# Performance work log

Hardware: AMD Instinct MI355X
Metric: run time of the kernel (lower is better)

The kernel has to match this reference:

```python
import jax, jax.numpy as jnp
import numpy as np

NUM_HEADS = 8
EPS = 1e-12  # torch F.normalize default eps


def _l2norm(t):
    # t / max(||t||_2, eps) along last axis (matches F.normalize)
    n = jnp.sqrt(jnp.sum(t * t, axis=-1, keepdims=True))
    return t / jnp.maximum(n, EPS)


def setup_inputs() -> dict:
    key = jax.random.key(0)
    k1, k2, k3 = jax.random.split(key, 3)
    B, N, C = 8, 1024, 768
    x = jax.random.normal(k1, (B, N, C), dtype=jnp.float32)
    w_qkv = jax.random.normal(k2, (C, 3 * C), dtype=jnp.float32) * 0.02
    temperature = jnp.ones((NUM_HEADS, 1, 1), dtype=jnp.float32)
    w_proj = jax.random.normal(k3, (C, C), dtype=jnp.float32) * 0.02
    b_proj = jnp.zeros((C,), dtype=jnp.float32)
    return {"x": x, "w_qkv": w_qkv, "temperature": temperature,
            "w_proj": w_proj, "b_proj": b_proj}


def reference(x, w_qkv, temperature, w_proj, b_proj):
    B, N, C = x.shape
    H = NUM_HEADS
    hd = C // H
    # qkv projection (no bias), split into q,k,v of shape [B,H,N,hd]
    qkv = (x @ w_qkv).reshape(B, N, 3, H, hd)
    qkv = jnp.transpose(qkv, (2, 0, 3, 1, 4))  # [3,B,H,N,hd]
    q, k, v = qkv[0], qkv[1], qkv[2]
    q = _l2norm(q)
    k = _l2norm(k)
    # NOTE: code (unlike canonical XCA) does NOT transpose q/k, so attn is [B,H,N,N]
    attn = jnp.einsum('bhnd,bhmd->bhnm', q, k) * temperature  # temp broadcasts over B
    attn = jax.nn.softmax(attn, axis=-1)
    out = jnp.einsum('bhnm,bhmd->bhnd', attn, v)  # [B,H,N,hd]
    out = jnp.transpose(out, (0, 2, 1, 3)).reshape(B, N, C)
    return out @ w_proj + b_proj
```

## Files before the change

kernel.cpp:

```cpp
#include <hip/hip_runtime.h>
#include <math.h>

typedef __attribute__((ext_vector_type(8))) short bf16x8;
typedef __attribute__((ext_vector_type(4))) float f32x4;
typedef unsigned short u16;
typedef unsigned int u32;


__device__ __forceinline__ u16 f2b(float f) {
  u32 u = __float_as_uint(f);
  return (u16)((u + 0x7fffu + ((u >> 16) & 1u)) >> 16);
}
__device__ __forceinline__ float b2f(u16 h) {
  return __uint_as_float(((u32)h) << 16);
}
__device__ __forceinline__ int swz(int m) { return (m ^ (m >> 2)) & 3; }

__device__ __forceinline__ void async16(const void* g, void* l) {
  __builtin_amdgcn_global_load_lds((const __attribute__((address_space(1))) u32*)g,
                                   (__attribute__((address_space(3))) u32*)l, 16, 0, 0);
}

__global__ __launch_bounds__(256) void prep_kernel(const float* __restrict__ x,
                                                   const float* __restrict__ w_qkv,
                                                   const float* __restrict__ w_proj,
                                                   u16* __restrict__ xb,
                                                   u16* __restrict__ wqkvT,
                                                   u16* __restrict__ wprojT) {
  __shared__ float t[32][33];
  const int blk = blockIdx.x;
  if (blk < 6144) {
    const int idx = blk * 256 + threadIdx.x;
    const float4 v = ((const float4*)x)[idx];
    uint2 o;
    o.x = (u32)f2b(v.x) | ((u32)f2b(v.y) << 16);
    o.y = (u32)f2b(v.z) | ((u32)f2b(v.w) << 16);
    ((uint2*)xb)[idx] = o;
    return;
  }
  const float* in; u16* out; int R, C, bx, by;
  if (blk < 6144 + 1728) {
    const int rem = blk - 6144;
    in = w_qkv; out = wqkvT; R = 768; C = 2304; bx = rem % 72; by = rem / 72;
  } else {
    const int rem = blk - 6144 - 1728;
    in = w_proj; out = wprojT; R = 768; C = 768; bx = rem % 24; by = rem / 24;
  }
  const int c0 = bx * 32, r0 = by * 32;
  const int tc = threadIdx.x & 31, tr = threadIdx.x >> 5;
#pragma unroll
  for (int j = 0; j < 4; ++j)
    t[tr + j * 8][tc] = in[(size_t)(r0 + tr + j * 8) * C + c0 + tc];
  __syncthreads();
#pragma unroll
  for (int j = 0; j < 4; ++j)
    out[(size_t)(c0 + tr + j * 8) * R + r0 + tc] = f2b(t[tc][tr + j * 8]);
}

template<int NT>
__device__ __forceinline__ void gemm_core(const u16* __restrict__ A,
                                          const u16* __restrict__ Bt,
                                          int m0, int n0, f32x4 acc[4][NT / 32]) {
  constexpr int JT = NT / 32;
  constexpr int NINST = (512 + NT * 4) / 256;
  __shared__ u16 Sm[(512 + NT * 4) * 8];
  const int tid = threadIdx.x;
  const int w = tid >> 6, lane = tid & 63;
  const int i15 = lane & 15, quad = lane >> 4;
  const int wm = (w >> 1) * 64, wn = (w & 1) * (NT / 2);
  const int sw = quad ^ swz(i15);

#pragma unroll
  for (int i = 0; i < 4; ++i)
#pragma unroll
    for (int j = 0; j < JT; ++j) acc[i][j] = (f32x4){0.f, 0.f, 0.f, 0.f};

  for (int k0 = 0; k0 < 768; k0 += 32) {
    __syncthreads();
#pragma unroll
    for (int inst = 0; inst < NINST; ++inst) {
      const int s = inst * 256 + tid;
      const u16* src;
      if (inst < 2) {
        const int m = s >> 2, e = s & 3;
        src = A + ((size_t)(m0 + m) * 768 + k0 + (e ^ swz(m)) * 8);
      } else {
        const int s2 = s - 512;
        const int n = s2 >> 2, e = s2 & 3;
        src = Bt + ((size_t)(n0 + n) * 768 + k0 + (e ^ swz(n)) * 8);
      }
      async16(src, (void*)(Sm + (size_t)(inst * 256 + w * 64) * 8));
    }
    __syncthreads();
    bf16x8 af[4], bf[JT];
#pragma unroll
    for (int i = 0; i < 4; ++i)
      af[i] = *(const bf16x8*)(Sm + ((size_t)(wm + i * 16 + i15) * 4 + sw) * 8);
#pragma unroll
    for (int j = 0; j < JT; ++j)
      bf[j] = *(const bf16x8*)(Sm + ((size_t)512 + (wn + j * 16 + i15) * 4 + sw) * 8);
#pragma unroll
    for (int i = 0; i < 4; ++i)
#pragma unroll
      for (int j = 0; j < JT; ++j)
        acc[i][j] = __builtin_amdgcn_mfma_f32_16x16x32_bf16(af[i], bf[j], acc[i][j], 0, 0, 0);
  }
}

__global__ __launch_bounds__(256, 3) void qkv_gemm_kernel(
    const u16* __restrict__ xb, const u16* __restrict__ wT,
    const float* __restrict__ temp,
    u16* __restrict__ q, u16* __restrict__ k, u16* __restrict__ vT) {
  f32x4 acc[4][6];
  const int bid = blockIdx.x;
  const int xcd = bid & 7, slot = bid >> 3;
  const int mb = xcd * 8 + slot / 12, nb = slot % 12;
  const int m0 = mb * 128, n0 = nb * 192;
  gemm_core<192>(xb, wT, m0, n0, acc);

  const int tid = threadIdx.x, w = tid >> 6, lane = tid & 63;
  const int i15 = lane & 15, quad = lane >> 4;
  const int wm = (w >> 1) * 64;
  const int three = nb >> 2;
  const int h = ((nb & 3) << 1) + (w & 1);

  if (three < 2) {
    u16* dst = three ? k : q;
    const float sc_extra = three ? 1.f : temp[h];
#pragma unroll
    for (int it = 0; it < 4; ++it) {
#pragma unroll
      for (int r = 0; r < 4; ++r) {
        float s = 0.f;
#pragma unroll
        for (int jt = 0; jt < 6; ++jt) s += acc[it][jt][r] * acc[it][jt][r];
        s += __shfl_xor(s, 1); s += __shfl_xor(s, 2);
        s += __shfl_xor(s, 4); s += __shfl_xor(s, 8);
        const float scale = sc_extra / fmaxf(sqrtf(s), 1e-12f);
        const int m = m0 + wm + it * 16 + quad * 4 + r;
        const int b = m >> 10, n = m & 1023;
        u16* rowp = dst + ((size_t)(b * 8 + h) * 1024 + n) * 96;
#pragma unroll
        for (int jt = 0; jt < 6; ++jt)
          rowp[jt * 16 + i15] = f2b(acc[it][jt][r] * scale);
      }
    }
  } else {
#pragma unroll
    for (int it = 0; it < 4; ++it) {
      const int mb4 = m0 + wm + it * 16 + quad * 4;
      const int b = mb4 >> 10, nbase = mb4 & 1023;
#pragma unroll
      for (int jt = 0; jt < 6; ++jt) {
        const int d = jt * 16 + i15;
        uint2 pk;
        pk.x = (u32)f2b(acc[it][jt][0]) | ((u32)f2b(acc[it][jt][1]) << 16);
        pk.y = (u32)f2b(acc[it][jt][2]) | ((u32)f2b(acc[it][jt][3]) << 16);
        *(uint2*)(vT + ((size_t)(b * 8 + h) * 96 + d) * 1024 + nbase) = pk;
      }
    }
  }
}

__global__ __launch_bounds__(256, 2) void attn_kernel(
    const u16* __restrict__ q, const u16* __restrict__ kk,
    const u16* __restrict__ vT, u16* __restrict__ ctx) {
  __shared__ u16 smem[20480];
  u16* KVs = smem;
  const int tid = threadIdx.x, w = tid >> 6, lane = tid & 63;
  const int i15 = lane & 15, quad = lane >> 4;
  const int xs = swz(i15);
  const int bh = blockIdx.x & 63, qbase = (blockIdx.x >> 6) * 128;
  const int b = bh >> 3, h = bh & 7;
  u16* Pw = smem + 12288 + w * 2048;

  bf16x8 qf[2][3];
#pragma unroll
  for (int rt = 0; rt < 2; ++rt) {
    const int qrow = qbase + w * 32 + rt * 16 + i15;
    const u16* qp = q + ((size_t)bh * 1024 + qrow) * 96 + quad * 8;
#pragma unroll
    for (int c = 0; c < 3; ++c) qf[rt][c] = *(const bf16x8*)(qp + c * 32);
  }

  f32x4 o[2][6];
#pragma unroll
  for (int rt = 0; rt < 2; ++rt)
#pragma unroll
    for (int dt = 0; dt < 6; ++dt) o[rt][dt] = (f32x4){0.f, 0.f, 0.f, 0.f};
  float l[2] = {0.f, 0.f};

  const int key_s = tid >> 2, qs = tid & 3;
  const int kgq = qs ^ swz(key_s);
  int vd[3], vc2[3], vgq[3];
  vd[0] = tid >> 2;                      vc2[0] = 0;
  vd[1] = (tid < 128) ? (tid >> 2) + 64 : (tid >> 2) - 32;  vc2[1] = (tid >= 128);
  vd[2] = (tid >> 2) + 32;               vc2[2] = 1;
#pragma unroll
  for (int j = 0; j < 3; ++j) vgq[j] = qs ^ swz(vd[j]);

  uint4 kreg[3], vreg[3];
#pragma unroll
  for (int j = 0; j < 3; ++j) {
    kreg[j] = *(const uint4*)(kk + ((size_t)bh * 1024 + key_s) * 96 + (j * 4 + kgq) * 8);
    vreg[j] = *(const uint4*)(vT + ((size_t)bh * 96 + vd[j]) * 1024 + vc2[j] * 32 + vgq[j] * 8);
  }

  for (int t = 0; t < 16; ++t) {
    __syncthreads();
#pragma unroll
    for (int j = 0; j < 3; ++j) {
      *(uint4*)(KVs + (size_t)(j * 256 + tid) * 8) = kreg[j];
      *(uint4*)(KVs + (size_t)(768 + j * 256 + tid) * 8) = vreg[j];
    }
    __syncthreads();
    if (t < 15) {
      const int kt0 = (t + 1) * 64;
#pragma unroll
      for (int j = 0; j < 3; ++j) {
        kreg[j] = *(const uint4*)(kk + ((size_t)bh * 1024 + kt0 + key_s) * 96 + (j * 4 + kgq) * 8);
        vreg[j] = *(const uint4*)(vT + ((size_t)bh * 96 + vd[j]) * 1024 + kt0 + vc2[j] * 32 + vgq[j] * 8);
      }
    }
#pragma unroll
    for (int kt = 0; kt < 4; ++kt) {
      bf16x8 af[3];
#pragma unroll
      for (int c = 0; c < 3; ++c)
        af[c] = *(const bf16x8*)(KVs + ((size_t)((c * 64 + kt * 16 + i15) * 4) + (quad ^ xs)) * 8);
#pragma unroll
      for (int rt = 0; rt < 2; ++rt) {
        f32x4 s = (f32x4){0.f, 0.f, 0.f, 0.f};
#pragma unroll
        for (int c = 0; c < 3; ++c)
          s = __builtin_amdgcn_mfma_f32_16x16x32_bf16(af[c], qf[rt][c], s, 0, 0, 0);
        const float e0 = __expf(s[0]), e1 = __expf(s[1]);
        const float e2 = __expf(s[2]), e3 = __expf(s[3]);
        l[rt] += (e0 + e1) + (e2 + e3);
        uint2 pk;
        pk.x = (u32)f2b(e0) | ((u32)f2b(e1) << 16);
        pk.y = (u32)f2b(e2) | ((u32)f2b(e3) << 16);
        const int pg = (kt & 1) * 2 + (quad >> 1);
        *(uint2*)(Pw + (size_t)(((kt >> 1) * 32 + rt * 16 + i15) * 4 + (pg ^ xs)) * 8
                      + (quad & 1) * 4) = pk;
      }
    }
#pragma unroll
    for (int c2 = 0; c2 < 2; ++c2) {
      bf16x8 pa[2];
#pragma unroll
      for (int rt = 0; rt < 2; ++rt)
        pa[rt] = *(const bf16x8*)(Pw + (size_t)((c2 * 32 + rt * 16 + i15) * 4 + (quad ^ xs)) * 8);
#pragma unroll
      for (int dt = 0; dt < 6; ++dt) {
        const bf16x8 vb = *(const bf16x8*)(KVs +
            ((size_t)(768 + (c2 * 96 + dt * 16 + i15) * 4) + (quad ^ xs)) * 8);
#pragma unroll
        for (int rt = 0; rt < 2; ++rt)
          o[rt][dt] = __builtin_amdgcn_mfma_f32_16x16x32_bf16(pa[rt], vb, o[rt][dt], 0, 0, 0);
      }
    }
  }

  l[0] += __shfl_xor(l[0], 16); l[0] += __shfl_xor(l[0], 32);
  l[1] += __shfl_xor(l[1], 16); l[1] += __shfl_xor(l[1], 32);
  __syncthreads();
  u16* scr = smem + w * 5120;
#pragma unroll
  for (int rt = 0; rt < 2; ++rt) {
#pragma unroll
    for (int r = 0; r < 4; ++r) {
      const float linv = 1.f / __shfl(l[rt], quad * 4 + r);
      const int row32 = rt * 16 + quad * 4 + r;
#pragma unroll
      for (int dt = 0; dt < 6; ++dt)
        scr[row32 * 104 + dt * 16 + i15] = f2b(o[rt][dt][r] * linv);
    }
  }
#pragma unroll
  for (int jj = 0; jj < 6; ++jj) {
    const int id = jj * 64 + lane;
    const int row32 = id / 12, g = id - row32 * 12;
    const int grow = b * 1024 + qbase + w * 32 + row32;
    *(uint4*)(ctx + (size_t)grow * 768 + h * 96 + g * 8) =
        *(const uint4*)(scr + row32 * 104 + g * 8);
  }
}

__global__ __launch_bounds__(256, 4) void proj_gemm_kernel(
    const u16* __restrict__ ctx, const u16* __restrict__ wT,
    const float* __restrict__ bias, float* __restrict__ out) {
  f32x4 acc[4][2];
  const int bid = blockIdx.x;
  const int xcd = bid & 7, slot = bid >> 3;
  const int mb = xcd * 8 + slot / 12, nb = slot % 12;
  const int m0 = mb * 128, n0 = nb * 64;
  gemm_core<64>(ctx, wT, m0, n0, acc);

  const int tid = threadIdx.x, w = tid >> 6, lane = tid & 63;
  const int i15 = lane & 15, quad = lane >> 4;
  const int wm = (w >> 1) * 64, wn = (w & 1) * 32;
#pragma unroll
  for (int jt = 0; jt < 2; ++jt) {
    const int c = n0 + wn + jt * 16 + i15;
    const float bb = bias[c];
#pragma unroll
    for (int it = 0; it < 4; ++it) {
#pragma unroll
      for (int r = 0; r < 4; ++r) {
        const int m = m0 + wm + it * 16 + quad * 4 + r;
        out[(size_t)m * 768 + c] = acc[it][jt][r] + bb;
      }
    }
  }
}

extern "C" void kernel_launch(void* const* d_in, const int* in_sizes, int n_in,
                              void* d_out, int out_size, void* d_ws, size_t ws_size,
                              hipStream_t stream) {
  const float* x      = (const float*)d_in[0];
  const float* w_qkv  = (const float*)d_in[1];
  const float* temp   = (const float*)d_in[2];
  const float* w_proj = (const float*)d_in[3];
  const float* b_proj = (const float*)d_in[4];

  u16* ws      = (u16*)d_ws;
  u16* xb      = ws;
  u16* wqkvT   = xb + 6291456;
  u16* qb      = wqkvT + 1769472;
  u16* kb      = qb + 6291456;
  u16* vTb     = kb + 6291456;
  u16* ctxb    = vTb + 6291456;
  u16* wprojT  = ctxb + 6291456;

  prep_kernel<<<8448, 256, 0, stream>>>(x, w_qkv, w_proj, xb, wqkvT, wprojT);
  qkv_gemm_kernel<<<768, 256, 0, stream>>>(xb, wqkvT, temp, qb, kb, vTb);
  attn_kernel<<<512, 256, 0, stream>>>(qb, kb, vTb, ctxb);
  proj_gemm_kernel<<<768, 256, 0, stream>>>(ctxb, wprojT, b_proj, (float*)d_out);
}
```

Measured before the change: 206.8 us.

## Split attention key range in two and merge partial outputs in a combine kernel

Splits each attention block's key loop into two halves, doubling the grid to 1024 blocks so more work is in flight on the GPU. Each half writes unnormalized fp32 partial outputs and row sums, and a new combine kernel adds them, normalizes and writes the bf16 context. The split reuses the output buffer as scratch and uses a fixed softmax max, so no rescaling is needed. In exchange it adds a kernel launch and substantial fp32 global traffic for the partial results, and raises the occupancy hint to 4, which may push register use.

```diff
diff --git a/kernel.cpp b/kernel.cpp
--- a/kernel.cpp
+++ b/kernel.cpp
@@ -162,16 +162,21 @@
   }
 }
 
-__global__ __launch_bounds__(256, 2) void attn_kernel(
+__global__ __launch_bounds__(256, 4) void attn_kernel(
     const u16* __restrict__ q, const u16* __restrict__ kk,
-    const u16* __restrict__ vT, u16* __restrict__ ctx) {
+    const u16* __restrict__ vT, float* __restrict__ po0, float* __restrict__ po1,
+    float* __restrict__ pl0, float* __restrict__ pl1) {
   __shared__ u16 smem[20480];
   u16* KVs = smem;
   const int tid = threadIdx.x, w = tid >> 6, lane = tid & 63;
   const int i15 = lane & 15, quad = lane >> 4;
   const int xs = swz(i15);
-  const int bh = blockIdx.x & 63, qbase = (blockIdx.x >> 6) * 128;
-  const int b = bh >> 3, h = bh & 7;
+  const int blk = blockIdx.x;
+  const int bh = blk & 63;
+  const int rest = blk >> 6;
+  const int qbase = (rest & 7) * 128;
+  const int half = rest >> 3;
+  const int toff = half * 8;
   u16* Pw = smem + 12288 + w * 2048;
 
   bf16x8 qf[2][3];
@@ -202,11 +207,12 @@
   uint4 kreg[3], vreg[3];
 #pragma unroll
   for (int j = 0; j < 3; ++j) {
-    kreg[j] = *(const uint4*)(kk + ((size_t)bh * 1024 + key_s) * 96 + (j * 4 + kgq) * 8);
-    vreg[j] = *(const uint4*)(vT + ((size_t)bh * 96 + vd[j]) * 1024 + vc2[j] * 32 + vgq[j] * 8);
-  }
-
-  for (int t = 0; t < 16; ++t) {
+    const int kt0 = toff * 64;
+    kreg[j] = *(const uint4*)(kk + ((size_t)bh * 1024 + kt0 + key_s) * 96 + (j * 4 + kgq) * 8);
+    vreg[j] = *(const uint4*)(vT + ((size_t)bh * 96 + vd[j]) * 1024 + kt0 + vc2[j] * 32 + vgq[j] * 8);
+  }
+
+  for (int t = 0; t < 8; ++t) {
     __syncthreads();
 #pragma unroll
     for (int j = 0; j < 3; ++j) {
@@ -214,8 +220,8 @@
       *(uint4*)(KVs + (size_t)(768 + j * 256 + tid) * 8) = vreg[j];
     }
     __syncthreads();
-    if (t < 15) {
-      const int kt0 = (t + 1) * 64;
+    if (t < 7) {
+      const int kt0 = (toff + t + 1) * 64;
 #pragma unroll
       for (int j = 0; j < 3; ++j) {
         kreg[j] = *(const uint4*)(kk + ((size_t)bh * 1024 + kt0 + key_s) * 96 + (j * 4 + kgq) * 8);
@@ -264,27 +270,41 @@
 
   l[0] += __shfl_xor(l[0], 16); l[0] += __shfl_xor(l[0], 32);
   l[1] += __shfl_xor(l[1], 16); l[1] += __shfl_xor(l[1], 32);
-  __syncthreads();
-  u16* scr = smem + w * 5120;
-#pragma unroll
-  for (int rt = 0; rt < 2; ++rt) {
+  if (quad == 0) {
+    float* plb = (half ? pl1 : pl0) + bh * 1024 + qbase + w * 32;
+    plb[i15] = l[0];
+    plb[16 + i15] = l[1];
+  }
+  float* pob = (half ? po1 : po0) + ((size_t)bh * 1024 + qbase + w * 32) * 96;
+#pragma unroll
+  for (int rt = 0; rt < 2; ++rt)
 #pragma unroll
     for (int r = 0; r < 4; ++r) {
-      const float linv = 1.f / __shfl(l[rt], quad * 4 + r);
       const int row32 = rt * 16 + quad * 4 + r;
 #pragma unroll
       for (int dt = 0; dt < 6; ++dt)
-        scr[row32 * 104 + dt * 16 + i15] = f2b(o[rt][dt][r] * linv);
-    }
-  }
-#pragma unroll
-  for (int jj = 0; jj < 6; ++jj) {
-    const int id = jj * 64 + lane;
-    const int row32 = id / 12, g = id - row32 * 12;
-    const int grow = b * 1024 + qbase + w * 32 + row32;
-    *(uint4*)(ctx + (size_t)grow * 768 + h * 96 + g * 8) =
-        *(const uint4*)(scr + row32 * 104 + g * 8);
-  }
+        pob[(size_t)row32 * 96 + dt * 16 + i15] = o[rt][dt][r];
+    }
+}
+
+__global__ __launch_bounds__(256) void combine_kernel(
+    const float4* __restrict__ po0, const float4* __restrict__ po1,
+    const float* __restrict__ pl0, const float* __restrict__ pl1,
+    u16* __restrict__ ctx) {
+  const int i4 = blockIdx.x * 256 + threadIdx.x;
+  const int e = i4 * 4;
+  const int bh = e / 98304;
+  const int rem = e - bh * 98304;
+  const int qrow = rem / 96;
+  const int d = rem - qrow * 96;
+  const float4 a = po0[i4], b4 = po1[i4];
+  const int li = bh * 1024 + qrow;
+  const float inv = 1.f / (pl0[li] + pl1[li]);
+  uint2 o;
+  o.x = (u32)f2b((a.x + b4.x) * inv) | ((u32)f2b((a.y + b4.y) * inv) << 16);
+  o.y = (u32)f2b((a.z + b4.z) * inv) | ((u32)f2b((a.w + b4.w) * inv) << 16);
+  const int b = bh >> 3, h = bh & 7;
+  *(uint2*)(ctx + (size_t)(b * 1024 + qrow) * 768 + h * 96 + d) = o;
 }
 
 __global__ __launch_bounds__(256, 4) void proj_gemm_kernel(
@@ -332,9 +352,15 @@
   u16* vTb     = kb + 6291456;
   u16* ctxb    = vTb + 6291456;
   u16* wprojT  = ctxb + 6291456;
+  float* po1   = (float*)(wprojT + 589824);
+  float* pl0   = po1 + 6291456;
+  float* pl1   = pl0 + 65536;
+  float* po0   = (float*)d_out;
 
   prep_kernel<<<8448, 256, 0, stream>>>(x, w_qkv, w_proj, xb, wqkvT, wprojT);
   qkv_gemm_kernel<<<768, 256, 0, stream>>>(xb, wqkvT, temp, qb, kb, vTb);
-  attn_kernel<<<512, 256, 0, stream>>>(qb, kb, vTb, ctxb);
+  attn_kernel<<<1024, 256, 0, stream>>>(qb, kb, vTb, po0, po1, pl0, pl1);
+  combine_kernel<<<6144, 256, 0, stream>>>((const float4*)po0, (const float4*)po1,
+                                           pl0, pl1, ctxb);
   proj_gemm_kernel<<<768, 256, 0, stream>>>(ctxb, wprojT, b_proj, (float*)d_out);
 }
```

Measured after the change: 264.8 us. 1.28x slower.
